# Optimization experiments

Measured on AMD Instinct MI355X. Metric: run time of the kernel, lower is better.

The kernel has to match this reference:

```python
import jax, jax.numpy as jnp
import numpy as np

B, K, SD, NA = 2, 512, 60, 5
E, H, D, FF, NL = 256, 4, 64, 1024, 2
EPS_F = 1e-6   # feature_eps in phi(x)=relu(x)+eps
LN_EPS = 1e-5  # torch LayerNorm default eps


def setup_inputs() -> dict:
    key = jax.random.key(0)
    ks = jax.random.split(key, 16)
    f = lambda i, shape, s=0.02: jax.random.normal(ks[i], shape, dtype=jnp.float32) * s
    return {
        "rtg": jax.random.normal(ks[0], (B, K, 1), dtype=jnp.float32),
        "state": jax.random.normal(ks[1], (B, K, SD), dtype=jnp.float32),
        "action": jax.random.normal(ks[2], (B, K, NA), dtype=jnp.float32),
        "rtg_w": f(3, (1, E)), "rtg_b": jnp.zeros((E,), jnp.float32),
        "state_w": f(4, (SD, E)), "state_b": jnp.zeros((E,), jnp.float32),
        "action_w": f(5, (NA, E)), "action_b": jnp.zeros((E,), jnp.float32),
        "pos_emb": f(6, (K, E)),
        "norm1_g": jnp.ones((NL, E), jnp.float32), "norm1_b": jnp.zeros((NL, E), jnp.float32),
        "qkv_w": f(7, (NL, E, 3 * E)), "qkv_b": jnp.zeros((NL, 3 * E), jnp.float32),
        "out_w": f(8, (NL, E, E)), "out_b": jnp.zeros((NL, E), jnp.float32),
        "norm2_g": jnp.ones((NL, E), jnp.float32), "norm2_b": jnp.zeros((NL, E), jnp.float32),
        "ffn1_w": f(9, (NL, E, FF)), "ffn1_b": jnp.zeros((NL, FF), jnp.float32),
        "ffn2_w": f(10, (NL, FF, E)), "ffn2_b": jnp.zeros((NL, E), jnp.float32),
        "normf_g": jnp.ones((E,), jnp.float32), "normf_b": jnp.zeros((E,), jnp.float32),
        "pred_w": f(11, (E, NA)), "pred_b": jnp.zeros((NA,), jnp.float32),
    }


def _ln(x, g, b):
    m = x.mean(-1, keepdims=True)
    v = jnp.mean((x - m) ** 2, -1, keepdims=True)
    return (x - m) * jax.lax.rsqrt(v + LN_EPS) * g + b


def _attn(x, qkv_w, qkv_b, out_w, out_b):
    b, l, _ = x.shape
    qkv = (x @ qkv_w + qkv_b).reshape(b, l, 3, H, D).transpose(2, 0, 3, 1, 4)
    q, k, v = qkv[0], qkv[1], qkv[2]          # each (b,h,l,d)
    q = jax.nn.relu(q) + EPS_F
    k = jax.nn.relu(k) + EPS_F
    kv = jnp.cumsum(jnp.einsum('bhld,bhle->bhlde', k, v), axis=2)  # (b,h,l,d,e)
    kcum = jnp.cumsum(k, axis=2)
    num = jnp.einsum('bhld,bhlde->bhle', q, kv)
    den = jnp.maximum(jnp.einsum('bhld,bhld->bhl', q, kcum)[..., None], 1e-6)
    o = (num / den).transpose(0, 2, 1, 3).reshape(b, l, H * D)
    return o @ out_w + out_b


def reference(rtg, state, action, rtg_w, rtg_b, state_w, state_b, action_w, action_b,
              pos_emb, norm1_g, norm1_b, qkv_w, qkv_b, out_w, out_b,
              norm2_g, norm2_b, ffn1_w, ffn1_b, ffn2_w, ffn2_b,
              normf_g, normf_b, pred_w, pred_b):
    b, k, _ = state.shape
    p = pos_emb[:k][None]
    r = rtg @ rtg_w + rtg_b + p
    s = state @ state_w + state_b + p
    a = action @ action_w + action_b + p
    # interleave (r,s,a) per timestep -> (b, 3k, E)
    x = jnp.stack((r, s, a), axis=2).reshape(b, 3 * k, E)
    for i in range(NL):
        x = x + _attn(_ln(x, norm1_g[i], norm1_b[i]), qkv_w[i], qkv_b[i], out_w[i], out_b[i])
        h = _ln(x, norm2_g[i], norm2_b[i])
        h = jax.nn.gelu(h @ ffn1_w[i] + ffn1_b[i], approximate=False) @ ffn2_w[i] + ffn2_b[i]
        x = x + h
    x = _ln(x, normf_g, normf_b)
    return x[:, 1::3, :] @ pred_w + pred_b  # predict from state tokens -> (b,k,num_actions)
```

## Files before the change

kernel.cpp:

```cpp
#include <hip/hip_runtime.h>
#include <hip/hip_bf16.h>
#include <math.h>

#define B_  2
#define K_  512
#define SD_ 60
#define NA_ 5
#define E_  256
#define H_  4
#define D_  64
#define FF_ 1024
#define NL_ 2
#define L_  (3 * K_)
#define M_  (B_ * L_)
#define EPS_F 1e-6f
#define LN_EPS 1e-5f
#define CHK 64
#define NC_ (L_ / CHK)

using bf16x8 = __attribute__((ext_vector_type(8))) short;
using f32x4  = __attribute__((ext_vector_type(4))) float;
typedef unsigned short u16;

__device__ inline u16 f2b(float v) {
    __hip_bfloat16 h = __float2bfloat16(v);
    return *(u16*)&h;
}
__device__ inline float b2f(u16 v) {
    __hip_bfloat16 h = *(__hip_bfloat16*)&v;
    return __bfloat162float(h);
}

__global__ __launch_bounds__(256) void init_kernel(
    const float* __restrict__ qkv_w, const float* __restrict__ out_w,
    const float* __restrict__ ffn1_w, const float* __restrict__ ffn2_w,
    u16* __restrict__ qkvT, u16* __restrict__ outT,
    u16* __restrict__ f1T, u16* __restrict__ f2T,
    const float* __restrict__ rtg, const float* __restrict__ state,
    const float* __restrict__ action,
    const float* __restrict__ rtg_w, const float* __restrict__ rtg_b,
    const float* __restrict__ state_w, const float* __restrict__ state_b,
    const float* __restrict__ action_w, const float* __restrict__ action_b,
    const float* __restrict__ pos,
    const float* __restrict__ g, const float* __restrict__ bta,
    float* __restrict__ X, u16* __restrict__ Y)
{
    __shared__ u16 T[32][33];
    if (blockIdx.x < 1536) {
        int tb = blockIdx.x;
        int layer = tb / 768;
        int r = tb % 768;
        const float* src; u16* dst; int K, N, tidx;
        if (r < 192)      { src = qkv_w  + layer * 196608; dst = qkvT + layer * 196608; K = 256;  N = 768;  tidx = r; }
        else if (r < 256) { src = out_w  + layer * 65536;  dst = outT + layer * 65536;  K = 256;  N = 256;  tidx = r - 192; }
        else if (r < 512) { src = ffn1_w + layer * 262144; dst = f1T  + layer * 262144; K = 256;  N = 1024; tidx = r - 256; }
        else              { src = ffn2_w + layer * 262144; dst = f2T  + layer * 262144; K = 1024; N = 256;  tidx = r - 512; }
        int tilesN = N >> 5;
        int k0 = (tidx / tilesN) << 5;
        int n0 = (tidx % tilesN) << 5;
        int c = threadIdx.x & 31, r0 = threadIdx.x >> 5;
        for (int rr = r0; rr < 32; rr += 8)
            T[rr][c] = f2b(src[(size_t)(k0 + rr) * N + n0 + c]);
        __syncthreads();
        for (int rr = r0; rr < 32; rr += 8)
            dst[(size_t)(n0 + rr) * K + k0 + c] = T[c][rr];
        return;
    }
    int tok = (blockIdx.x - 1536) * 4 + (threadIdx.x >> 6);
    int lane = threadIdx.x & 63;
    int b = tok / L_, l = tok % L_;
    int j = l % 3, t = l / 3;
    int e0 = lane * 4;
    float4 val = *(const float4*)(pos + t * E_ + e0);
    if (j == 0) {
        float rv = rtg[b * K_ + t];
        float4 w = *(const float4*)(rtg_w + e0);
        float4 bb = *(const float4*)(rtg_b + e0);
        val.x += rv * w.x + bb.x; val.y += rv * w.y + bb.y;
        val.z += rv * w.z + bb.z; val.w += rv * w.w + bb.w;
    } else if (j == 1) {
        float4 a = *(const float4*)(state_b + e0);
        const float* srow = state + ((size_t)b * K_ + t) * SD_;
        for (int i = 0; i < SD_; i++) {
            float s = srow[i];
            float4 w = *(const float4*)(state_w + (size_t)i * E_ + e0);
            a.x += s * w.x; a.y += s * w.y; a.z += s * w.z; a.w += s * w.w;
        }
        val.x += a.x; val.y += a.y; val.z += a.z; val.w += a.w;
    } else {
        float4 a = *(const float4*)(action_b + e0);
        const float* arow = action + ((size_t)b * K_ + t) * NA_;
        #pragma unroll
        for (int i = 0; i < NA_; i++) {
            float s = arow[i];
            float4 w = *(const float4*)(action_w + (size_t)i * E_ + e0);
            a.x += s * w.x; a.y += s * w.y; a.z += s * w.z; a.w += s * w.w;
        }
        val.x += a.x; val.y += a.y; val.z += a.z; val.w += a.w;
    }
    *(float4*)(X + (size_t)tok * E_ + e0) = val;
    float s = val.x + val.y + val.z + val.w;
    #pragma unroll
    for (int o = 32; o; o >>= 1) s += __shfl_xor(s, o, 64);
    float mean = s * (1.f / E_);
    float dx = val.x - mean, dy = val.y - mean, dz = val.z - mean, dw = val.w - mean;
    float q = dx * dx + dy * dy + dz * dz + dw * dw;
    #pragma unroll
    for (int o = 32; o; o >>= 1) q += __shfl_xor(q, o, 64);
    float inv = rsqrtf(q * (1.f / E_) + LN_EPS);
    float4 gv = *(const float4*)(g + e0);
    float4 bv = *(const float4*)(bta + e0);
    ushort4 u;
    u.x = f2b(dx * inv * gv.x + bv.x); u.y = f2b(dy * inv * gv.y + bv.y);
    u.z = f2b(dz * inv * gv.z + bv.z); u.w = f2b(dw * inv * gv.w + bv.w);
    *(ushort4*)(Y + (size_t)tok * E_ + e0) = u;
}

__global__ __launch_bounds__(256) void ln_kernel(
    const float* __restrict__ X, const float* __restrict__ g,
    const float* __restrict__ b, u16* __restrict__ Y)
{
    int tok = blockIdx.x * 4 + (threadIdx.x >> 6);
    int lane = threadIdx.x & 63;
    int e0 = lane * 4;
    float4 v = *(const float4*)(X + (size_t)tok * E_ + e0);
    float s = v.x + v.y + v.z + v.w;
    #pragma unroll
    for (int o = 32; o; o >>= 1) s += __shfl_xor(s, o, 64);
    float mean = s * (1.f / E_);
    float dx = v.x - mean, dy = v.y - mean, dz = v.z - mean, dw = v.w - mean;
    float q = dx * dx + dy * dy + dz * dz + dw * dw;
    #pragma unroll
    for (int o = 32; o; o >>= 1) q += __shfl_xor(q, o, 64);
    float inv = rsqrtf(q * (1.f / E_) + LN_EPS);
    float4 gv = *(const float4*)(g + e0);
    float4 bv = *(const float4*)(b + e0);
    ushort4 u;
    u.x = f2b(dx * inv * gv.x + bv.x); u.y = f2b(dy * inv * gv.y + bv.y);
    u.z = f2b(dz * inv * gv.z + bv.z); u.w = f2b(dw * inv * gv.w + bv.w);
    *(ushort4*)(Y + (size_t)tok * E_ + e0) = u;
}

template <int EPI>
__global__ __launch_bounds__(256) void mgemm(
    const u16* __restrict__ A, const u16* __restrict__ Bt,
    const float* __restrict__ bias,
    u16* __restrict__ C, int M, int N, int Kd)
{
    __shared__ __align__(16) u16 As[2][128 * 40];
    __shared__ __align__(16) u16 Bs[2][128 * 40];
    int tid = threadIdx.x;
    int bm = blockIdx.y * 128, bn = blockIdx.x * 128;
    int wave = tid >> 6, lane = tid & 63;
    int wm = (wave >> 1) * 64, wn = (wave & 1) * 64;
    int lr = lane & 15, kg = lane >> 4;

    int r0 = tid >> 2, g0 = (tid & 3) * 8;
    int r1 = r0 + 64;

    const u16* Ap0 = A + (size_t)(bm + r0) * Kd + g0;
    const u16* Ap1 = A + (size_t)(bm + r1) * Kd + g0;
    const u16* Bp0 = Bt + (size_t)(bn + r0) * Kd + g0;
    const u16* Bp1 = Bt + (size_t)(bn + r1) * Kd + g0;

    uint4 a0 = *(const uint4*)(Ap0);
    uint4 a1 = *(const uint4*)(Ap1);
    uint4 b0 = *(const uint4*)(Bp0);
    uint4 b1 = *(const uint4*)(Bp1);
    *(uint4*)&As[0][r0 * 40 + g0] = a0;
    *(uint4*)&As[0][r1 * 40 + g0] = a1;
    *(uint4*)&Bs[0][r0 * 40 + g0] = b0;
    *(uint4*)&Bs[0][r1 * 40 + g0] = b1;

    f32x4 acc[4][4] = {};
    int NT = Kd >> 5;
    for (int t = 0; t < NT; ++t) {
        int cur = t & 1;
        __syncthreads();
        if (t + 1 < NT) {
            int k1 = (t + 1) << 5;
            a0 = *(const uint4*)(Ap0 + k1);
            a1 = *(const uint4*)(Ap1 + k1);
            b0 = *(const uint4*)(Bp0 + k1);
            b1 = *(const uint4*)(Bp1 + k1);
        }
        bf16x8 af[4], bg[4];
        #pragma unroll
        for (int i = 0; i < 4; i++)
            af[i] = *(const bf16x8*)&As[cur][(wm + i * 16 + lr) * 40 + kg * 8];
        #pragma unroll
        for (int j = 0; j < 4; j++)
            bg[j] = *(const bf16x8*)&Bs[cur][(wn + j * 16 + lr) * 40 + kg * 8];
        #pragma unroll
        for (int i = 0; i < 4; i++)
            #pragma unroll
            for (int j = 0; j < 4; j++)
                acc[i][j] = __builtin_amdgcn_mfma_f32_16x16x32_bf16(
                    af[i], bg[j], acc[i][j], 0, 0, 0);
        if (t + 1 < NT) {
            *(uint4*)&As[cur ^ 1][r0 * 40 + g0] = a0;
            *(uint4*)&As[cur ^ 1][r1 * 40 + g0] = a1;
            *(uint4*)&Bs[cur ^ 1][r0 * 40 + g0] = b0;
            *(uint4*)&Bs[cur ^ 1][r1 * 40 + g0] = b1;
        }
    }

    #pragma unroll
    for (int i = 0; i < 4; i++) {
        #pragma unroll
        for (int j = 0; j < 4; j++) {
            int col = bn + wn + j * 16 + lr;
            float bc = bias[col];
            #pragma unroll
            for (int r = 0; r < 4; r++) {
                int row = bm + wm + i * 16 + kg * 4 + r;
                float v = acc[i][j][r] + bc;
                if (EPI == 1) v = 0.5f * v * (1.0f + erff(v * 0.70710678118654752f));
                C[(size_t)row * N + col] = f2b(v);
            }
        }
    }
}

__global__ __launch_bounds__(256) void gemm64res(
    const u16* __restrict__ A, const u16* __restrict__ Bt,
    const float* __restrict__ bias, float* __restrict__ X, int Kd)
{
    __shared__ __align__(16) u16 As[2][64 * 72];
    __shared__ __align__(16) u16 Bs[2][64 * 72];
    int tid = threadIdx.x;
    int tile = blockIdx.x;
    int bm = (tile >> 2) * 64, bn = (tile & 3) * 64;
    int wave = tid >> 6, lane = tid & 63;
    int wm = (wave >> 1) * 32, wn = (wave & 1) * 32;
    int lr = lane & 15, kg = lane >> 4;
    int r = tid >> 2, c8 = (tid & 3) * 8;

    const u16* Ap = A + (size_t)(bm + r) * Kd + c8;
    const u16* Bp = Bt + (size_t)(bn + r) * Kd + c8;

    uint4 a0 = *(const uint4*)(Ap);
    uint4 a1 = *(const uint4*)(Ap + 32);
    uint4 b0 = *(const uint4*)(Bp);
    uint4 b1 = *(const uint4*)(Bp + 32);
    *(uint4*)&As[0][r * 72 + c8]      = a0;
    *(uint4*)&As[0][r * 72 + 32 + c8] = a1;
    *(uint4*)&Bs[0][r * 72 + c8]      = b0;
    *(uint4*)&Bs[0][r * 72 + 32 + c8] = b1;

    f32x4 acc[2][2] = {};
    int NT = Kd >> 6;
    for (int t = 0; t < NT; ++t) {
        int cur = t & 1;
        __syncthreads();
        if (t + 1 < NT) {
            int k1 = (t + 1) << 6;
            a0 = *(const uint4*)(Ap + k1);
            a1 = *(const uint4*)(Ap + k1 + 32);
            b0 = *(const uint4*)(Bp + k1);
            b1 = *(const uint4*)(Bp + k1 + 32);
        }
        bf16x8 af0[2], af1[2], bg0[2], bg1[2];
        #pragma unroll
        for (int i = 0; i < 2; i++) {
            af0[i] = *(const bf16x8*)&As[cur][(wm + i * 16 + lr) * 72 + kg * 8];
            af1[i] = *(const bf16x8*)&As[cur][(wm + i * 16 + lr) * 72 + 32 + kg * 8];
        }
        #pragma unroll
        for (int j = 0; j < 2; j++) {
            bg0[j] = *(const bf16x8*)&Bs[cur][(wn + j * 16 + lr) * 72 + kg * 8];
            bg1[j] = *(const bf16x8*)&Bs[cur][(wn + j * 16 + lr) * 72 + 32 + kg * 8];
        }
        #pragma unroll
        for (int i = 0; i < 2; i++)
            #pragma unroll
            for (int j = 0; j < 2; j++) {
                acc[i][j] = __builtin_amdgcn_mfma_f32_16x16x32_bf16(
                    af0[i], bg0[j], acc[i][j], 0, 0, 0);
                acc[i][j] = __builtin_amdgcn_mfma_f32_16x16x32_bf16(
                    af1[i], bg1[j], acc[i][j], 0, 0, 0);
            }
        if (t + 1 < NT) {
            *(uint4*)&As[cur ^ 1][r * 72 + c8]      = a0;
            *(uint4*)&As[cur ^ 1][r * 72 + 32 + c8] = a1;
            *(uint4*)&Bs[cur ^ 1][r * 72 + c8]      = b0;
            *(uint4*)&Bs[cur ^ 1][r * 72 + 32 + c8] = b1;
        }
    }
    #pragma unroll
    for (int i = 0; i < 2; i++) {
        #pragma unroll
        for (int j = 0; j < 2; j++) {
            int col = bn + wn + j * 16 + lr;
            float bc = bias[col];
            #pragma unroll
            for (int rr = 0; rr < 4; rr++) {
                int row = bm + wm + i * 16 + kg * 4 + rr;
                float v = acc[i][j][rr] + bc + X[(size_t)row * 256 + col];
                X[(size_t)row * 256 + col] = v;
            }
        }
    }
}

__global__ __launch_bounds__(256) void chunk_sum_kernel(
    const u16* __restrict__ QKV, float* __restrict__ S, float* __restrict__ Z)
{
    int blk = blockIdx.x;
    int c = blk % NC_;
    int bh = blk / NC_;
    int h = bh % H_;
    int b = bh / H_;
    __shared__ __align__(16) u16 Kt[64 * 72];
    __shared__ __align__(16) u16 Vt[64 * 72];
    int tid = threadIdx.x;
    const size_t base = ((size_t)b * L_ + (size_t)c * CHK) * 768 + h * 64;
    for (int i = tid; i < 1024; i += 256) {
        int t = i >> 4, d4 = (i & 15) << 2;
        ushort4 k = *(const ushort4*)(QKV + base + (size_t)t * 768 + 256 + d4);
        ushort4 v = *(const ushort4*)(QKV + base + (size_t)t * 768 + 512 + d4);
        Kt[(d4 + 0) * 72 + t] = f2b(fmaxf(b2f(k.x), 0.f) + EPS_F);
        Kt[(d4 + 1) * 72 + t] = f2b(fmaxf(b2f(k.y), 0.f) + EPS_F);
        Kt[(d4 + 2) * 72 + t] = f2b(fmaxf(b2f(k.z), 0.f) + EPS_F);
        Kt[(d4 + 3) * 72 + t] = f2b(fmaxf(b2f(k.w), 0.f) + EPS_F);
        Vt[(d4 + 0) * 72 + t] = v.x;
        Vt[(d4 + 1) * 72 + t] = v.y;
        Vt[(d4 + 2) * 72 + t] = v.z;
        Vt[(d4 + 3) * 72 + t] = v.w;
    }
    __syncthreads();
    int wave = tid >> 6, lane = tid & 63;
    int lr = lane & 15, kg = lane >> 4;
    int wm = wave * 16;
    bf16x8 a0 = *(const bf16x8*)&Kt[(wm + lr) * 72 + kg * 8];
    bf16x8 a1 = *(const bf16x8*)&Kt[(wm + lr) * 72 + 32 + kg * 8];
    f32x4 acc[4] = {};
    #pragma unroll
    for (int j = 0; j < 4; j++) {
        bf16x8 b0 = *(const bf16x8*)&Vt[(j * 16 + lr) * 72 + kg * 8];
        bf16x8 b1 = *(const bf16x8*)&Vt[(j * 16 + lr) * 72 + 32 + kg * 8];
        acc[j] = __builtin_amdgcn_mfma_f32_16x16x32_bf16(a0, b0, acc[j], 0, 0, 0);
        acc[j] = __builtin_amdgcn_mfma_f32_16x16x32_bf16(a1, b1, acc[j], 0, 0, 0);
    }
    if (tid < 64) {
        float z = 0.f;
        #pragma unroll 8
        for (int t = 0; t < 64; t++) z += b2f(Kt[tid * 72 + t]);
        Z[(size_t)blk * 64 + tid] = z;
    }
    float* Sp = S + (size_t)blk * 4096;
    #pragma unroll
    for (int j = 0; j < 4; j++) {
        #pragma unroll
        for (int rr = 0; rr < 4; rr++) {
            int d = wm + kg * 4 + rr;
            int e = j * 16 + lr;
            Sp[d * 64 + e] = acc[j][rr];
        }
    }
}

__global__ __launch_bounds__(256) void chunk_out_kernel(
    const u16* __restrict__ QKV, const float* __restrict__ S,
    const float* __restrict__ Z, u16* __restrict__ O)
{
    int blk = blockIdx.x;
    int c = blk % NC_;
    int bh = blk / NC_;
    int h = bh % H_;
    int b = bh / H_;
    __shared__ __align__(16) u16 Qb[64 * 72];
    __shared__ __align__(16) u16 Kb[64 * 72];
    __shared__ __align__(16) u16 Vt[64 * 72];
    __shared__ __align__(16) u16 KVt[64 * 72];
    __shared__ __align__(16) u16 Ps[64 * 72];
    __shared__ float kzs[64];
    __shared__ float rows[64];
    __shared__ float invs[64];
    int tid = threadIdx.x;
    const size_t base = ((size_t)b * L_ + (size_t)c * CHK) * 768 + h * 64;
    const float* Sbh = S + (size_t)bh * NC_ * 4096;
    for (int i = tid; i < 1024; i += 256) {
        int t = i >> 4, d4 = (i & 15) << 2;
        ushort4 q = *(const ushort4*)(QKV + base + (size_t)t * 768 + d4);
        ushort4 k = *(const ushort4*)(QKV + base + (size_t)t * 768 + 256 + d4);
        ushort4 v = *(const ushort4*)(QKV + base + (size_t)t * 768 + 512 + d4);
        ushort4 qu, ku;
        qu.x = f2b(fmaxf(b2f(q.x), 0.f) + EPS_F); qu.y = f2b(fmaxf(b2f(q.y), 0.f) + EPS_F);
        qu.z = f2b(fmaxf(b2f(q.z), 0.f) + EPS_F); qu.w = f2b(fmaxf(b2f(q.w), 0.f) + EPS_F);
        ku.x = f2b(fmaxf(b2f(k.x), 0.f) + EPS_F); ku.y = f2b(fmaxf(b2f(k.y), 0.f) + EPS_F);
        ku.z = f2b(fmaxf(b2f(k.z), 0.f) + EPS_F); ku.w = f2b(fmaxf(b2f(k.w), 0.f) + EPS_F);
        *(ushort4*)&Qb[t * 72 + d4] = qu;
        *(ushort4*)&Kb[t * 72 + d4] = ku;
        Vt[(d4 + 0) * 72 + t] = v.x;
        Vt[(d4 + 1) * 72 + t] = v.y;
        Vt[(d4 + 2) * 72 + t] = v.z;
        Vt[(d4 + 3) * 72 + t] = v.w;
        int d = t, e4 = d4;
        float4 a = make_float4(0.f, 0.f, 0.f, 0.f);
        for (int cc = 0; cc < c; cc++) {
            float4 s4 = *(const float4*)(Sbh + (size_t)cc * 4096 + d * 64 + e4);
            a.x += s4.x; a.y += s4.y; a.z += s4.z; a.w += s4.w;
        }
        KVt[(e4 + 0) * 72 + d] = f2b(a.x);
        KVt[(e4 + 1) * 72 + d] = f2b(a.y);
        KVt[(e4 + 2) * 72 + d] = f2b(a.z);
        KVt[(e4 + 3) * 72 + d] = f2b(a.w);
    }
    if (tid < 64) {
        float z = 0.f;
        const float* Zbh = Z + (size_t)bh * NC_ * 64;
        for (int cc = 0; cc < c; cc++) z += Zbh[cc * 64 + tid];
        kzs[tid] = z;
    }
    __syncthreads();

    int wave = tid >> 6, lane = tid & 63;
    int lr = lane & 15, kg = lane >> 4;
    int wm = wave * 16;

    bf16x8 aq0 = *(const bf16x8*)&Qb[(wm + lr) * 72 + kg * 8];
    bf16x8 aq1 = *(const bf16x8*)&Qb[(wm + lr) * 72 + 32 + kg * 8];

    f32x4 accs[4] = {};
    #pragma unroll
    for (int j = 0; j < 4; j++) {
        bf16x8 b0 = *(const bf16x8*)&Kb[(j * 16 + lr) * 72 + kg * 8];
        bf16x8 b1 = *(const bf16x8*)&Kb[(j * 16 + lr) * 72 + 32 + kg * 8];
        accs[j] = __builtin_amdgcn_mfma_f32_16x16x32_bf16(aq0, b0, accs[j], 0, 0, 0);
        accs[j] = __builtin_amdgcn_mfma_f32_16x16x32_bf16(aq1, b1, accs[j], 0, 0, 0);
    }
    float rsum[4] = {0.f, 0.f, 0.f, 0.f};
    #pragma unroll
    for (int j = 0; j < 4; j++) {
        #pragma unroll
        for (int rr = 0; rr < 4; rr++) {
            int m = wm + kg * 4 + rr;
            int n = j * 16 + lr;
            float v = (n <= m) ? accs[j][rr] : 0.f;
            rsum[rr] += v;
            Ps[m * 72 + n] = f2b(v);
        }
    }
    #pragma unroll
    for (int rr = 0; rr < 4; rr++) {
        float s = rsum[rr];
        s += __shfl_xor(s, 1, 64);
        s += __shfl_xor(s, 2, 64);
        s += __shfl_xor(s, 4, 64);
        s += __shfl_xor(s, 8, 64);
        if (lr == 0) rows[wm + kg * 4 + rr] = s;
    }
    __syncthreads();

    if (tid < 64) {
        float den = rows[tid];
        float acc = 0.f;
        #pragma unroll 8
        for (int d = 0; d < 64; d++) acc += b2f(Qb[tid * 72 + d]) * kzs[d];
        invs[tid] = 1.f / fmaxf(den + acc, 1e-6f);
    }

    bf16x8 ap0 = *(const bf16x8*)&Ps[(wm + lr) * 72 + kg * 8];
    bf16x8 ap1 = *(const bf16x8*)&Ps[(wm + lr) * 72 + 32 + kg * 8];
    f32x4 accn[4] = {};
    #pragma unroll
    for (int j = 0; j < 4; j++) {
        bf16x8 b0 = *(const bf16x8*)&KVt[(j * 16 + lr) * 72 + kg * 8];
        bf16x8 b1 = *(const bf16x8*)&KVt[(j * 16 + lr) * 72 + 32 + kg * 8];
        accn[j] = __builtin_amdgcn_mfma_f32_16x16x32_bf16(aq0, b0, accn[j], 0, 0, 0);
        accn[j] = __builtin_amdgcn_mfma_f32_16x16x32_bf16(aq1, b1, accn[j], 0, 0, 0);
        bf16x8 c0 = *(const bf16x8*)&Vt[(j * 16 + lr) * 72 + kg * 8];
        bf16x8 c1 = *(const bf16x8*)&Vt[(j * 16 + lr) * 72 + 32 + kg * 8];
        accn[j] = __builtin_amdgcn_mfma_f32_16x16x32_bf16(ap0, c0, accn[j], 0, 0, 0);
        accn[j] = __builtin_amdgcn_mfma_f32_16x16x32_bf16(ap1, c1, accn[j], 0, 0, 0);
    }
    __syncthreads();

    u16* Op = O + ((size_t)b * L_ + (size_t)c * CHK) * E_ + h * 64;
    #pragma unroll
    for (int j = 0; j < 4; j++) {
        #pragma unroll
        for (int rr = 0; rr < 4; rr++) {
            int m = wm + kg * 4 + rr;
            int e = j * 16 + lr;
            Op[(size_t)m * E_ + e] = f2b(accn[j][rr] * invs[m]);
        }
    }
}

__global__ __launch_bounds__(256) void lnpred_kernel(
    const float* __restrict__ X, const float* __restrict__ g,
    const float* __restrict__ bt, const float* __restrict__ W,
    const float* __restrict__ bias, float* __restrict__ Out)
{
    int si = blockIdx.x * 4 + (threadIdx.x >> 6);
    int lane = threadIdx.x & 63;
    int b = si / K_, t = si % K_;
    size_t row = (size_t)b * L_ + 3 * t + 1;
    int e0 = lane * 4;
    float4 v = *(const float4*)(X + row * E_ + e0);
    float s = v.x + v.y + v.z + v.w;
    #pragma unroll
    for (int o = 32; o; o >>= 1) s += __shfl_xor(s, o, 64);
    float mean = s * (1.f / E_);
    float dx = v.x - mean, dy = v.y - mean, dz = v.z - mean, dw = v.w - mean;
    float q = dx * dx + dy * dy + dz * dz + dw * dw;
    #pragma unroll
    for (int o = 32; o; o >>= 1) q += __shfl_xor(q, o, 64);
    float inv = rsqrtf(q * (1.f / E_) + LN_EPS);
    float4 gv = *(const float4*)(g + e0);
    float4 bv = *(const float4*)(bt + e0);
    float y0 = dx * inv * gv.x + bv.x;
    float y1 = dy * inv * gv.y + bv.y;
    float y2 = dz * inv * gv.z + bv.z;
    float y3 = dw * inv * gv.w + bv.w;
    #pragma unroll
    for (int na = 0; na < NA_; na++) {
        float a = y0 * W[(e0 + 0) * NA_ + na] + y1 * W[(e0 + 1) * NA_ + na]
                + y2 * W[(e0 + 2) * NA_ + na] + y3 * W[(e0 + 3) * NA_ + na];
        #pragma unroll
        for (int o = 32; o; o >>= 1) a += __shfl_xor(a, o, 64);
        if (lane == 0) Out[(size_t)si * NA_ + na] = a + bias[na];
    }
}

extern "C" void kernel_launch(void* const* d_in, const int* in_sizes, int n_in,
                              void* d_out, int out_size, void* d_ws, size_t ws_size,
                              hipStream_t stream) {
    const float* rtg      = (const float*)d_in[0];
    const float* state    = (const float*)d_in[1];
    const float* action   = (const float*)d_in[2];
    const float* rtg_w    = (const float*)d_in[3];
    const float* rtg_b    = (const float*)d_in[4];
    const float* state_w  = (const float*)d_in[5];
    const float* state_b  = (const float*)d_in[6];
    const float* action_w = (const float*)d_in[7];
    const float* action_b = (const float*)d_in[8];
    const float* pos_emb  = (const float*)d_in[9];
    const float* norm1_g  = (const float*)d_in[10];
    const float* norm1_b  = (const float*)d_in[11];
    const float* qkv_w    = (const float*)d_in[12];
    const float* qkv_b    = (const float*)d_in[13];
    const float* out_w    = (const float*)d_in[14];
    const float* out_b    = (const float*)d_in[15];
    const float* norm2_g  = (const float*)d_in[16];
    const float* norm2_b  = (const float*)d_in[17];
    const float* ffn1_w   = (const float*)d_in[18];
    const float* ffn1_b   = (const float*)d_in[19];
    const float* ffn2_w   = (const float*)d_in[20];
    const float* ffn2_b   = (const float*)d_in[21];
    const float* normf_g  = (const float*)d_in[22];
    const float* normf_b  = (const float*)d_in[23];
    const float* pred_w   = (const float*)d_in[24];
    const float* pred_b   = (const float*)d_in[25];
    float* out = (float*)d_out;

    float* ws = (float*)d_ws;
    float* x    = ws;
    float* S    = x + 786432;
    float* Z    = S + 786432;
    u16*   yb   = (u16*)(Z + 12288);
    u16*   qkvb = yb + 786432;
    u16*   att  = qkvb + 2359296;
    u16*   h1   = att + 786432;
    u16*   qkvT = h1 + 3145728;
    u16*   outT = qkvT + 393216;
    u16*   f1T  = outT + 131072;
    u16*   f2T  = f1T + 524288;

    init_kernel<<<2304, 256, 0, stream>>>(
        qkv_w, out_w, ffn1_w, ffn2_w, qkvT, outT, f1T, f2T,
        rtg, state, action, rtg_w, rtg_b, state_w, state_b,
        action_w, action_b, pos_emb, norm1_g, norm1_b, x, yb);

    for (int i = 0; i < NL_; i++) {
        mgemm<0><<<dim3(768 / 128, M_ / 128), 256, 0, stream>>>(
            yb, qkvT + (size_t)i * 196608, qkv_b + i * 768, qkvb,
            M_, 768, E_);
        chunk_sum_kernel<<<B_ * H_ * NC_, 256, 0, stream>>>(qkvb, S, Z);
        chunk_out_kernel<<<B_ * H_ * NC_, 256, 0, stream>>>(qkvb, S, Z, att);
        gemm64res<<<M_ / 64 * 4, 256, 0, stream>>>(
            att, outT + (size_t)i * 65536, out_b + i * E_, x, E_);
        ln_kernel<<<M_ / 4, 256, 0, stream>>>(
            x, norm2_g + i * E_, norm2_b + i * E_, yb);
        mgemm<1><<<dim3(FF_ / 128, M_ / 128), 256, 0, stream>>>(
            yb, f1T + (size_t)i * 262144, ffn1_b + i * FF_, h1,
            M_, FF_, E_);
        gemm64res<<<M_ / 64 * 4, 256, 0, stream>>>(
            h1, f2T + (size_t)i * 262144, ffn2_b + i * E_, x, FF_);
        if (i == 0)
            ln_kernel<<<M_ / 4, 256, 0, stream>>>(
                x, norm1_g + E_, norm1_b + E_, yb);
    }
    lnpred_kernel<<<(B_ * K_) / 4, 256, 0, stream>>>(
        x, normf_g, normf_b, pred_w, pred_b, out);
}
```

Baseline: 259.2 us.

## Fuse chunk-sum and chunk-output attention kernels with inter-block flag synchronization

Merges the two linear-attention chunk kernels into one launch. Each block publishes its chunk K^T V and K-sum state to global memory, sets a release flag, and spins until all earlier chunks of the same batch-head have published before doing the prefix accumulation. The relu+eps feature map on q and k moves into the QKV GEMM epilogue, so the attention kernel stages raw tiles. This removes one launch and repeated QKV loads. In exchange it depends on all 96 blocks being resident at once to avoid deadlock, and adds spin-wait latency plus a flag-reset block in init.

After: 297.7 us. +14.9%, slower.

```diff
diff --git a/kernel.cpp b/kernel.cpp
--- a/kernel.cpp
+++ b/kernel.cpp
@@ -43,9 +43,14 @@
     const float* __restrict__ action_w, const float* __restrict__ action_b,
     const float* __restrict__ pos,
     const float* __restrict__ g, const float* __restrict__ bta,
-    float* __restrict__ X, u16* __restrict__ Y)
+    float* __restrict__ X, u16* __restrict__ Y,
+    unsigned* __restrict__ flags)
 {
     __shared__ u16 T[32][33];
+    if (blockIdx.x >= 2304) {
+        if (threadIdx.x < 192) flags[threadIdx.x] = 0u;
+        return;
+    }
     if (blockIdx.x < 1536) {
         int tb = blockIdx.x;
         int layer = tb / 768;
@@ -216,6 +221,7 @@
                 int row = bm + wm + i * 16 + kg * 4 + r;
                 float v = acc[i][j][r] + bc;
                 if (EPI == 1) v = 0.5f * v * (1.0f + erff(v * 0.70710678118654752f));
+                if (EPI == 2) { if (col < 512) v = fmaxf(v, 0.f) + EPS_F; }
                 C[(size_t)row * N + col] = f2b(v);
             }
         }
@@ -303,66 +309,10 @@
     }
 }
 
-__global__ __launch_bounds__(256) void chunk_sum_kernel(
-    const u16* __restrict__ QKV, float* __restrict__ S, float* __restrict__ Z)
-{
-    int blk = blockIdx.x;
-    int c = blk % NC_;
-    int bh = blk / NC_;
-    int h = bh % H_;
-    int b = bh / H_;
-    __shared__ __align__(16) u16 Kt[64 * 72];
-    __shared__ __align__(16) u16 Vt[64 * 72];
-    int tid = threadIdx.x;
-    const size_t base = ((size_t)b * L_ + (size_t)c * CHK) * 768 + h * 64;
-    for (int i = tid; i < 1024; i += 256) {
-        int t = i >> 4, d4 = (i & 15) << 2;
-        ushort4 k = *(const ushort4*)(QKV + base + (size_t)t * 768 + 256 + d4);
-        ushort4 v = *(const ushort4*)(QKV + base + (size_t)t * 768 + 512 + d4);
-        Kt[(d4 + 0) * 72 + t] = f2b(fmaxf(b2f(k.x), 0.f) + EPS_F);
-        Kt[(d4 + 1) * 72 + t] = f2b(fmaxf(b2f(k.y), 0.f) + EPS_F);
-        Kt[(d4 + 2) * 72 + t] = f2b(fmaxf(b2f(k.z), 0.f) + EPS_F);
-        Kt[(d4 + 3) * 72 + t] = f2b(fmaxf(b2f(k.w), 0.f) + EPS_F);
-        Vt[(d4 + 0) * 72 + t] = v.x;
-        Vt[(d4 + 1) * 72 + t] = v.y;
-        Vt[(d4 + 2) * 72 + t] = v.z;
-        Vt[(d4 + 3) * 72 + t] = v.w;
-    }
-    __syncthreads();
-    int wave = tid >> 6, lane = tid & 63;
-    int lr = lane & 15, kg = lane >> 4;
-    int wm = wave * 16;
-    bf16x8 a0 = *(const bf16x8*)&Kt[(wm + lr) * 72 + kg * 8];
-    bf16x8 a1 = *(const bf16x8*)&Kt[(wm + lr) * 72 + 32 + kg * 8];
-    f32x4 acc[4] = {};
-    #pragma unroll
-    for (int j = 0; j < 4; j++) {
-        bf16x8 b0 = *(const bf16x8*)&Vt[(j * 16 + lr) * 72 + kg * 8];
-        bf16x8 b1 = *(const bf16x8*)&Vt[(j * 16 + lr) * 72 + 32 + kg * 8];
-        acc[j] = __builtin_amdgcn_mfma_f32_16x16x32_bf16(a0, b0, acc[j], 0, 0, 0);
-        acc[j] = __builtin_amdgcn_mfma_f32_16x16x32_bf16(a1, b1, acc[j], 0, 0, 0);
-    }
-    if (tid < 64) {
-        float z = 0.f;
-        #pragma unroll 8
-        for (int t = 0; t < 64; t++) z += b2f(Kt[tid * 72 + t]);
-        Z[(size_t)blk * 64 + tid] = z;
-    }
-    float* Sp = S + (size_t)blk * 4096;
-    #pragma unroll
-    for (int j = 0; j < 4; j++) {
-        #pragma unroll
-        for (int rr = 0; rr < 4; rr++) {
-            int d = wm + kg * 4 + rr;
-            int e = j * 16 + lr;
-            Sp[d * 64 + e] = acc[j][rr];
-        }
-    }
-}
-
-__global__ __launch_bounds__(256) void chunk_out_kernel(
-    const u16* __restrict__ QKV, const float* __restrict__ S,
-    const float* __restrict__ Z, u16* __restrict__ O)
+__global__ __launch_bounds__(256) void chunk_fused(
+    const u16* __restrict__ QKV, float* __restrict__ S,
+    float* __restrict__ Z, unsigned* __restrict__ flags, int gen,
+    u16* __restrict__ O)
 {
     int blk = blockIdx.x;
     int c = blk % NC_;
@@ -371,6 +321,7 @@
     int b = bh / H_;
     __shared__ __align__(16) u16 Qb[64 * 72];
     __shared__ __align__(16) u16 Kb[64 * 72];
+    __shared__ __align__(16) u16 Kt[64 * 72];
     __shared__ __align__(16) u16 Vt[64 * 72];
     __shared__ __align__(16) u16 KVt[64 * 72];
     __shared__ __align__(16) u16 Ps[64 * 72];
@@ -379,24 +330,110 @@
     __shared__ float invs[64];
     int tid = threadIdx.x;
     const size_t base = ((size_t)b * L_ + (size_t)c * CHK) * 768 + h * 64;
-    const float* Sbh = S + (size_t)bh * NC_ * 4096;
+
     for (int i = tid; i < 1024; i += 256) {
         int t = i >> 4, d4 = (i & 15) << 2;
         ushort4 q = *(const ushort4*)(QKV + base + (size_t)t * 768 + d4);
         ushort4 k = *(const ushort4*)(QKV + base + (size_t)t * 768 + 256 + d4);
         ushort4 v = *(const ushort4*)(QKV + base + (size_t)t * 768 + 512 + d4);
-        ushort4 qu, ku;
-        qu.x = f2b(fmaxf(b2f(q.x), 0.f) + EPS_F); qu.y = f2b(fmaxf(b2f(q.y), 0.f) + EPS_F);
-        qu.z = f2b(fmaxf(b2f(q.z), 0.f) + EPS_F); qu.w = f2b(fmaxf(b2f(q.w), 0.f) + EPS_F);
-        ku.x = f2b(fmaxf(b2f(k.x), 0.f) + EPS_F); ku.y = f2b(fmaxf(b2f(k.y), 0.f) + EPS_F);
-        ku.z = f2b(fmaxf(b2f(k.z), 0.f) + EPS_F); ku.w = f2b(fmaxf(b2f(k.w), 0.f) + EPS_F);
-        *(ushort4*)&Qb[t * 72 + d4] = qu;
-        *(ushort4*)&Kb[t * 72 + d4] = ku;
+        *(ushort4*)&Qb[t * 72 + d4] = q;
+        *(ushort4*)&Kb[t * 72 + d4] = k;
+        Kt[(d4 + 0) * 72 + t] = k.x;
+        Kt[(d4 + 1) * 72 + t] = k.y;
+        Kt[(d4 + 2) * 72 + t] = k.z;
+        Kt[(d4 + 3) * 72 + t] = k.w;
         Vt[(d4 + 0) * 72 + t] = v.x;
         Vt[(d4 + 1) * 72 + t] = v.y;
         Vt[(d4 + 2) * 72 + t] = v.z;
         Vt[(d4 + 3) * 72 + t] = v.w;
-        int d = t, e4 = d4;
+    }
+    __syncthreads();
+
+    int wave = tid >> 6, lane = tid & 63;
+    int lr = lane & 15, kg = lane >> 4;
+    int wm = wave * 16;
+
+    {
+        bf16x8 a0 = *(const bf16x8*)&Kt[(wm + lr) * 72 + kg * 8];
+        bf16x8 a1 = *(const bf16x8*)&Kt[(wm + lr) * 72 + 32 + kg * 8];
+        f32x4 acc[4] = {};
+        #pragma unroll
+        for (int j = 0; j < 4; j++) {
+            bf16x8 b0 = *(const bf16x8*)&Vt[(j * 16 + lr) * 72 + kg * 8];
+            bf16x8 b1 = *(const bf16x8*)&Vt[(j * 16 + lr) * 72 + 32 + kg * 8];
+            acc[j] = __builtin_amdgcn_mfma_f32_16x16x32_bf16(a0, b0, acc[j], 0, 0, 0);
+            acc[j] = __builtin_amdgcn_mfma_f32_16x16x32_bf16(a1, b1, acc[j], 0, 0, 0);
+        }
+        if (tid < 64) {
+            float z = 0.f;
+            #pragma unroll 8
+            for (int t = 0; t < 64; t++) z += b2f(Kt[tid * 72 + t]);
+            Z[(size_t)blk * 64 + tid] = z;
+        }
+        float* Sp = S + (size_t)blk * 4096;
+        #pragma unroll
+        for (int j = 0; j < 4; j++) {
+            #pragma unroll
+            for (int rr = 0; rr < 4; rr++) {
+                int d = wm + kg * 4 + rr;
+                int e = j * 16 + lr;
+                Sp[d * 64 + e] = acc[j][rr];
+            }
+        }
+    }
+    __threadfence();
+    __syncthreads();
+    if (tid == 0)
+        __hip_atomic_store(&flags[blk], (unsigned)gen,
+                           __ATOMIC_RELEASE, __HIP_MEMORY_SCOPE_AGENT);
+
+    bf16x8 aq0 = *(const bf16x8*)&Qb[(wm + lr) * 72 + kg * 8];
+    bf16x8 aq1 = *(const bf16x8*)&Qb[(wm + lr) * 72 + 32 + kg * 8];
+    {
+        f32x4 accs[4] = {};
+        #pragma unroll
+        for (int j = 0; j < 4; j++) {
+            bf16x8 b0 = *(const bf16x8*)&Kb[(j * 16 + lr) * 72 + kg * 8];
+            bf16x8 b1 = *(const bf16x8*)&Kb[(j * 16 + lr) * 72 + 32 + kg * 8];
+            accs[j] = __builtin_amdgcn_mfma_f32_16x16x32_bf16(aq0, b0, accs[j], 0, 0, 0);
+            accs[j] = __builtin_amdgcn_mfma_f32_16x16x32_bf16(aq1, b1, accs[j], 0, 0, 0);
+        }
+        float rsum[4] = {0.f, 0.f, 0.f, 0.f};
+        #pragma unroll
+        for (int j = 0; j < 4; j++) {
+            #pragma unroll
+            for (int rr = 0; rr < 4; rr++) {
+                int m = wm + kg * 4 + rr;
+                int n = j * 16 + lr;
+                float v = (n <= m) ? accs[j][rr] : 0.f;
+                rsum[rr] += v;
+                Ps[m * 72 + n] = f2b(v);
+            }
+        }
+        #pragma unroll
+        for (int rr = 0; rr < 4; rr++) {
+            float s = rsum[rr];
+            s += __shfl_xor(s, 1, 64);
+            s += __shfl_xor(s, 2, 64);
+            s += __shfl_xor(s, 4, 64);
+            s += __shfl_xor(s, 8, 64);
+            if (lr == 0) rows[wm + kg * 4 + rr] = s;
+        }
+    }
+
+    if (tid < c) {
+        while (__hip_atomic_load(&flags[bh * NC_ + tid],
+                                 __ATOMIC_RELAXED, __HIP_MEMORY_SCOPE_AGENT)
+               < (unsigned)gen)
+            __builtin_amdgcn_s_sleep(2);
+    }
+    __syncthreads();
+    if (tid == 0) __threadfence();
+    __syncthreads();
+
+    const float* Sbh = S + (size_t)bh * NC_ * 4096;
+    for (int i = tid; i < 1024; i += 256) {
+        int d = i >> 4, e4 = (i & 15) << 2;
         float4 a = make_float4(0.f, 0.f, 0.f, 0.f);
         for (int cc = 0; cc < c; cc++) {
             float4 s4 = *(const float4*)(Sbh + (size_t)cc * 4096 + d * 64 + e4);
@@ -412,44 +449,6 @@
         const float* Zbh = Z + (size_t)bh * NC_ * 64;
         for (int cc = 0; cc < c; cc++) z += Zbh[cc * 64 + tid];
         kzs[tid] = z;
-    }
-    __syncthreads();
-
-    int wave = tid >> 6, lane = tid & 63;
-    int lr = lane & 15, kg = lane >> 4;
-    int wm = wave * 16;
-
-    bf16x8 aq0 = *(const bf16x8*)&Qb[(wm + lr) * 72 + kg * 8];
-    bf16x8 aq1 = *(const bf16x8*)&Qb[(wm + lr) * 72 + 32 + kg * 8];
-
-    f32x4 accs[4] = {};
-    #pragma unroll
-    for (int j = 0; j < 4; j++) {
-        bf16x8 b0 = *(const bf16x8*)&Kb[(j * 16 + lr) * 72 + kg * 8];
-        bf16x8 b1 = *(const bf16x8*)&Kb[(j * 16 + lr) * 72 + 32 + kg * 8];
-        accs[j] = __builtin_amdgcn_mfma_f32_16x16x32_bf16(aq0, b0, accs[j], 0, 0, 0);
-        accs[j] = __builtin_amdgcn_mfma_f32_16x16x32_bf16(aq1, b1, accs[j], 0, 0, 0);
-    }
-    float rsum[4] = {0.f, 0.f, 0.f, 0.f};
-    #pragma unroll
-    for (int j = 0; j < 4; j++) {
-        #pragma unroll
-        for (int rr = 0; rr < 4; rr++) {
-            int m = wm + kg * 4 + rr;
-            int n = j * 16 + lr;
-            float v = (n <= m) ? accs[j][rr] : 0.f;
-            rsum[rr] += v;
-            Ps[m * 72 + n] = f2b(v);
-        }
-    }
-    #pragma unroll
-    for (int rr = 0; rr < 4; rr++) {
-        float s = rsum[rr];
-        s += __shfl_xor(s, 1, 64);
-        s += __shfl_xor(s, 2, 64);
-        s += __shfl_xor(s, 4, 64);
-        s += __shfl_xor(s, 8, 64);
-        if (lr == 0) rows[wm + kg * 4 + rr] = s;
     }
     __syncthreads();
 
@@ -568,18 +567,19 @@
     u16*   outT = qkvT + 393216;
     u16*   f1T  = outT + 131072;
     u16*   f2T  = f1T + 524288;
-
-    init_kernel<<<2304, 256, 0, stream>>>(
+    unsigned* flags = (unsigned*)(f2T + 524288);
+
+    init_kernel<<<2305, 256, 0, stream>>>(
         qkv_w, out_w, ffn1_w, ffn2_w, qkvT, outT, f1T, f2T,
         rtg, state, action, rtg_w, rtg_b, state_w, state_b,
-        action_w, action_b, pos_emb, norm1_g, norm1_b, x, yb);
+        action_w, action_b, pos_emb, norm1_g, norm1_b, x, yb, flags);
 
     for (int i = 0; i < NL_; i++) {
-        mgemm<0><<<dim3(768 / 128, M_ / 128), 256, 0, stream>>>(
+        mgemm<2><<<dim3(768 / 128, M_ / 128), 256, 0, stream>>>(
             yb, qkvT + (size_t)i * 196608, qkv_b + i * 768, qkvb,
             M_, 768, E_);
-        chunk_sum_kernel<<<B_ * H_ * NC_, 256, 0, stream>>>(qkvb, S, Z);
-        chunk_out_kernel<<<B_ * H_ * NC_, 256, 0, stream>>>(qkvb, S, Z, att);
+        chunk_fused<<<B_ * H_ * NC_, 256, 0, stream>>>(
+            qkvb, S, Z, flags, i + 1, att);
         gemm64res<<<M_ / 64 * 4, 256, 0, stream>>>(
             att, outT + (size_t)i * 65536, out_b + i * E_, x, E_);
         ln_kernel<<<M_ / 4, 256, 0, stream>>>(
```
